# Optimization experiments

Hardware: AMD Instinct MI355X
Metric: run time of the kernel (lower is better)

The kernel has to match this reference:

```python
import jax, jax.numpy as jnp
import numpy as np
from jax import lax

B, W, L, E, V, C, H, O = 16384, 5, 20, 50, 100000, 128, 4096, 50


def setup_inputs() -> dict:
    key = jax.random.key(0)
    ks = jax.random.split(key, 10)
    x = jax.random.randint(ks[0], (B, W), 1, V)
    word_id_to_chars_ids = jax.random.randint(ks[1], (V, L), 0, C)
    word_emb = jax.random.normal(ks[2], (V, E), dtype=jnp.float32) * 0.1
    word_emb = word_emb.at[0].set(0.0)  # padding_idx=0
    char_emb = jax.random.normal(ks[3], (C, E), dtype=jnp.float32) * 0.1
    char_emb = char_emb.at[0].set(0.0)  # padding_idx=0
    conv_w = jax.random.normal(ks[4], (E, E, 3), dtype=jnp.float32) * (1.0 / np.sqrt(E * 3))
    conv_b = jax.random.normal(ks[5], (E,), dtype=jnp.float32) * 0.01
    fc1_w = jax.random.normal(ks[6], (H, E * W), dtype=jnp.float32) * (1.0 / np.sqrt(E * W))
    fc1_b = jnp.zeros((H,), dtype=jnp.float32)
    fc2_w = jax.random.normal(ks[7], (O, H), dtype=jnp.float32) * (1.0 / np.sqrt(H))
    fc2_b = jnp.zeros((O,), dtype=jnp.float32)
    return {"x": x, "word_id_to_chars_ids": word_id_to_chars_ids,
            "word_emb": word_emb, "char_emb": char_emb,
            "conv_w": conv_w, "conv_b": conv_b,
            "fc1_w": fc1_w, "fc1_b": fc1_b, "fc2_w": fc2_w, "fc2_b": fc2_b}


def reference(x, word_id_to_chars_ids, word_emb, char_emb, conv_w, conv_b,
              fc1_w, fc1_b, fc2_w, fc2_b):
    # per-window char ids: [B, 5, L] -> char embeddings [B, 5, L, E]
    char_ids = word_id_to_chars_ids[x]
    ce = char_emb[char_ids]
    # conv1d over char positions: reshape to NCW = [B*5, E, L]
    ce = ce.reshape(B * W, L, E).transpose(0, 2, 1)
    conv = lax.conv_general_dilated(ce, conv_w, window_strides=(1,),
                                    padding=[(1, 1)],
                                    dimension_numbers=("NCH", "OIH", "NCH"))
    conv = conv + conv_b[None, :, None]
    # max-pool over char positions (kernel == L): [B*5, E] -> [B, 5, E]
    chars = jnp.max(conv, axis=2).reshape(B, W, E)
    words = word_emb[x]  # [B, 5, E]
    h = (words + chars).reshape(B, W * E)  # view(-1, 250)
    h = jnp.tanh(h @ fc1_w.T + fc1_b)
    logits = h @ fc2_w.T + fc2_b
    return jax.nn.softmax(logits, axis=1)
```

## Files before the change

kernel.cpp:

```cpp
#include <hip/hip_runtime.h>
#include <hip/hip_bf16.h>


typedef __attribute__((ext_vector_type(8))) short short8;
typedef __attribute__((ext_vector_type(4))) float float4v;

__device__ inline short bf16b(float f) {
    __hip_bfloat16 h = __float2bfloat16(f);
    return *reinterpret_cast<short*>(&h);
}
__device__ inline uint packbf2(float a, float b) {
    return (uint)(ushort)bf16b(a) | ((uint)(ushort)bf16b(b) << 16);
}
__device__ inline void gload_lds16(const void* g, void* l) {
    __builtin_amdgcn_global_load_lds(
        (const __attribute__((address_space(1))) unsigned int*)g,
        (__attribute__((address_space(3))) unsigned int*)l, 16, 0, 0);
}

__global__ __launch_bounds__(256) void prep_kernel(
    const float* __restrict__ fc1_w, const float* __restrict__ fc1_b,
    const float* __restrict__ fc2_w, const float* __restrict__ char_emb,
    const float* __restrict__ conv_w, short* __restrict__ wbf,
    short* __restrict__ w2bf, float* __restrict__ gt2)
{
    const int bid = blockIdx.x;
    if (bid < 4096) {
        int idx = bid * 256 + threadIdx.x;
        int n = idx >> 8, k = idx & 255;
        float v = (k < 250) ? fc1_w[n * 250 + k] : (k == 250 ? fc1_b[n] : 0.f);
        int CT = n >> 4, mm = n & 15;
        int ks = k >> 5, qq = (k >> 3) & 3, j = k & 7;
        wbf[((CT * 8 + ks) * 64 + qq * 16 + mm) * 8 + j] = bf16b(v);
    } else if (bid < 5120) {
        int idx = (bid - 4096) * 256 + threadIdx.x;
        int o = idx >> 12, k = idx & 4095;
        float v = (o < 50) ? fc2_w[idx] : 0.f;
        int Ot = o >> 4, mm = o & 15;
        int kst = k >> 5, qq = (k >> 3) & 3, j = k & 7;
        w2bf[((kst * 4 + Ot) * 64 + qq * 16 + mm) * 8 + j] = bf16b(v);
    } else {
        int idx = (bid - 5120) * 256 + threadIdx.x;
        if (idx >= 19200) return;
        int c = idx / 150, rem = idx - c * 150;
        int kk = rem / 50, o = rem - kk * 50;
        const float* ce = char_emb + c * 50;
        const float* w  = conv_w + o * 150 + kk;
        float s = 0.f;
        #pragma unroll 10
        for (int i = 0; i < 50; ++i) s += ce[i] * w[i * 3];
        if (kk < 2) gt2[(c * 50 + o) * 2 + kk] = s;
        else        gt2[12800 + c * 50 + o] = s;
    }
}

__global__ __launch_bounds__(512, 1) void fused_kernel(
    const int* __restrict__ x, const int* __restrict__ wci,
    const float* __restrict__ word_emb, const float* __restrict__ conv_b,
    const float* __restrict__ gt2, const short* __restrict__ wbf,
    const short* __restrict__ w2bf, const float* __restrict__ fc2_b,
    float* __restrict__ out)
{
    __shared__ char smem[147456];
    short8* Bsv   = (short8*)smem;
    char*   hsb   = smem + 131072;
    float*  partf = (float*)smem;
    char*   gsb   = smem;
    uint*   cpackS = (uint*)(smem + 76800);
    int*    xsS    = (int*)(smem + 83200);
    char*   haS    = smem + 98304;

    const int tid  = threadIdx.x;
    const int lane = tid & 63;
    const int wv   = tid >> 6;
    const int wr = wv >> 2, wc = wv & 3;
    const int q = lane >> 4, m = lane & 15;
    const int m0 = blockIdx.x * 64;
    const int q2base = q >> 1, slot = q & 1;

    const short8* wbfv  = (const short8*)wbf;
    const short8* w2bfv = (const short8*)w2bf;

    {
        const float4* g4 = (const float4*)gt2;
        float4* s4 = (float4*)gsb;
        #pragma unroll
        for (int i = 0; i < 10; ++i) {
            int idx = i * 512 + tid;
            if (idx < 4800) s4[idx] = g4[idx];
        }
    }
    if (tid < 320) {
        const int xid = x[m0 * 5 + tid];
        xsS[tid] = xid;
        const int* crow = wci + (size_t)xid * 20;
        int cid[20];
        #pragma unroll
        for (int p = 0; p < 20; ++p) cid[p] = crow[p];
        #pragma unroll
        for (int u = 0; u < 5; ++u)
            cpackS[tid * 5 + u] = (uint)cid[u * 4] | ((uint)cid[u * 4 + 1] << 8)
                                | ((uint)cid[u * 4 + 2] << 16) | ((uint)cid[u * 4 + 3] << 24);
    }
    __syncthreads();

    {
        const int oc = (lane < 50) ? lane : 49;
        const float cbias = conv_b[oc];
        const int oc8 = oc * 8, oc4 = oc * 4;
        for (int i = 0; i < 40; ++i) {
            const int w = i * 8 + wv;
            const int xid = xsS[w];
            const float wer = word_emb[(size_t)xid * 50 + oc];
            uint cw[5];
            #pragma unroll
            for (int u = 0; u < 5; ++u) cw[u] = cpackS[w * 5 + u];
            int cc[20];
            #pragma unroll
            for (int p = 0; p < 20; ++p)
                cc[p] = (int)((cw[p >> 2] >> ((p & 3) * 8)) & 0xFF);

            float2 r01[11]; float r2[11];
            #pragma unroll
            for (int l = 0; l < 11; ++l) {
                r01[l] = *(const float2*)(gsb + cc[l] * 400 + oc8);
                r2[l]  = *(const float*)(gsb + 51200 + cc[l] * 200 + oc4);
            }
            float mx = r01[0].y + r2[1];
            #pragma unroll
            for (int l = 1; l < 10; ++l) {
                float s = r01[l].y + r01[l - 1].x + r2[l + 1];
                mx = fmaxf(mx, s);
            }
            const float2 r9 = r01[9], r10 = r01[10];

            float2 q01[9]; float q2v[9];
            #pragma unroll
            for (int l = 0; l < 9; ++l) {
                q01[l] = *(const float2*)(gsb + cc[11 + l] * 400 + oc8);
                q2v[l] = *(const float*)(gsb + 51200 + cc[11 + l] * 200 + oc4);
            }
            { float s = r10.y + r9.x + q2v[0];  mx = fmaxf(mx, s); }
            { float s = q01[0].y + r10.x + q2v[1]; mx = fmaxf(mx, s); }
            #pragma unroll
            for (int l = 12; l < 19; ++l) {
                float s = q01[l - 11].y + q01[l - 12].x + q2v[l - 10];
                mx = fmaxf(mx, s);
            }
            { float s = q01[8].y + q01[7].x; mx = fmaxf(mx, s); }

            if (lane < 50) {
                const int s = w / 5, wp = w - s * 5;
                const int byteoff = (s * 512 + (wp * 50 + oc) * 2) ^ ((s & 7) << 4);
                *(short*)(haS + byteoff) = bf16b(mx + cbias + wer);
            }
        }
    }
    if (tid < 384) {
        const int s = tid / 6, j = tid - s * 6;
        const int byteoff = (s * 512 + (250 + j) * 2) ^ ((s & 7) << 4);
        *(short*)(haS + byteoff) = bf16b(j == 0 ? 1.f : 0.f);
    }
    __syncthreads();

    short8 av[2][8];
    #pragma unroll
    for (int mt = 0; mt < 2; ++mt)
        #pragma unroll
        for (int ks = 0; ks < 8; ++ks) {
            const int r = wr * 32 + mt * 16 + m;
            const int byteoff = (r * 512 + ks * 64 + q * 16) ^ ((r & 7) << 4);
            av[mt][ks] = *(const short8*)(haS + byteoff);
        }
    #pragma unroll
    for (int mt = 0; mt < 2; ++mt)
        #pragma unroll
        for (int ks = 0; ks < 8; ++ks)
            asm volatile("" : "+v"(av[mt][ks]));
    __syncthreads();

    #pragma unroll
    for (int i = 0; i < 8; ++i)
        gload_lds16(wbfv + i * 512 + tid, Bsv + i * 512 + tid);
    __syncthreads();

    float4v acc2[2][4] = {};

    #pragma unroll 4
    for (int chg = 0; chg < 32; ++chg) {
        const int buf = chg & 1;

        short8 b2[4];
        #pragma unroll
        for (int Ot = 0; Ot < 4; ++Ot)
            b2[Ot] = w2bfv[(size_t)((chg * 4 + wc) * 4 + Ot) * 64 + lane];

        #pragma unroll
        for (int i = 0; i < 8; ++i)
            gload_lds16(wbfv + (size_t)(chg + 1) * 4096 + i * 512 + tid,
                        Bsv + (buf ^ 1) * 4096 + i * 512 + tid);

        float4v acc[2][2] = {};
        #pragma unroll
        for (int ks = 0; ks < 8; ++ks) {
            short8 bv[2];
            #pragma unroll
            for (int nt = 0; nt < 2; ++nt)
                bv[nt] = Bsv[buf * 4096 + ((wc * 2 + nt) * 8 + ks) * 64 + lane];
            #pragma unroll
            for (int mt = 0; mt < 2; ++mt)
                #pragma unroll
                for (int nt = 0; nt < 2; ++nt)
                    acc[mt][nt] = __builtin_amdgcn_mfma_f32_16x16x32_bf16(
                        bv[nt], av[mt][ks], acc[mt][nt], 0, 0, 0);
        }

        #pragma unroll
        for (int mt = 0; mt < 2; ++mt) {
            const int frag = (wr * 2 + mt) * 4 + wc;
            #pragma unroll
            for (int nt = 0; nt < 2; ++nt) {
                float tv[4];
                #pragma unroll
                for (int r = 0; r < 4; ++r)
                    tv[r] = 1.f - 2.f / (__expf(2.f * acc[mt][nt][r]) + 1.f);
                const int q2 = nt * 2 + q2base;
                const uint p0 = packbf2(tv[0], tv[1]);
                const uint p1 = packbf2(tv[2], tv[3]);
                *(uint2*)(hsb + ((frag * 64 + q2 * 16 + m) * 16 + slot * 8))
                    = make_uint2(p0, p1);
            }
        }

        {
            short8 a2[2];
            #pragma unroll
            for (int mt = 0; mt < 2; ++mt)
                a2[mt] = *(const short8*)(hsb
                    + (((wr * 2 + mt) * 4 + wc) * 64 + lane) * 16);
            #pragma unroll
            for (int mt = 0; mt < 2; ++mt)
                #pragma unroll
                for (int Ot = 0; Ot < 4; ++Ot)
                    acc2[mt][Ot] = __builtin_amdgcn_mfma_f32_16x16x32_bf16(
                        a2[mt], b2[Ot], acc2[mt][Ot], 0, 0, 0);
        }

        __syncthreads();
    }

    #pragma unroll
    for (int mt = 0; mt < 2; ++mt)
        #pragma unroll
        for (int Ot = 0; Ot < 4; ++Ot)
            #pragma unroll
            for (int r = 0; r < 4; ++r)
                partf[(size_t)wc * 4096
                      + ((wr * 2 + mt) * 16 + q * 4 + r) * 64 + Ot * 16 + m]
                    = acc2[mt][Ot][r];
    __syncthreads();

    #pragma unroll
    for (int t = 0; t < 8; ++t) {
        int idx = t * 512 + tid;
        int col = idx & 63;
        float lg = partf[idx] + partf[4096 + idx]
                 + partf[8192 + idx] + partf[12288 + idx];
        partf[idx] = (col < 50) ? lg + fc2_b[col] : -1e30f;
    }
    __syncthreads();

    #pragma unroll
    for (int rr = 0; rr < 8; ++rr) {
        const int row = wv * 8 + rr;
        float v = partf[row * 64 + lane];
        float mx = v;
        #pragma unroll
        for (int off = 32; off > 0; off >>= 1) mx = fmaxf(mx, __shfl_xor(mx, off));
        float e = __expf(v - mx);
        float s = e;
        #pragma unroll
        for (int off = 32; off > 0; off >>= 1) s += __shfl_xor(s, off);
        if (lane < 50)
            out[(size_t)(m0 + row) * 50 + lane] = e / s;
    }
}

extern "C" void kernel_launch(void* const* d_in, const int* in_sizes, int n_in,
                              void* d_out, int out_size, void* d_ws, size_t ws_size,
                              hipStream_t stream) {
    const int*   x        = (const int*)  d_in[0];
    const int*   wci      = (const int*)  d_in[1];
    const float* word_emb = (const float*)d_in[2];
    const float* char_emb = (const float*)d_in[3];
    const float* conv_w   = (const float*)d_in[4];
    const float* conv_b   = (const float*)d_in[5];
    const float* fc1_w    = (const float*)d_in[6];
    const float* fc1_b    = (const float*)d_in[7];
    const float* fc2_w    = (const float*)d_in[8];
    const float* fc2_b    = (const float*)d_in[9];
    float* out = (float*)d_out;

    char* ws = (char*)d_ws;
    short* wbf  = (short*)(ws + ((size_t)8  << 20));
    short* w2bf = (short*)(ws + ((size_t)10 << 20));
    float* gt2  = (float*)(ws + ((size_t)11 << 20));

    prep_kernel<<<5195, 256, 0, stream>>>(fc1_w, fc1_b, fc2_w, char_emb,
                                          conv_w, wbf, w2bf, gt2);
    fused_kernel<<<256, 512, 0, stream>>>(x, wci, word_emb, conv_b, gt2,
                                          wbf, w2bf, fc2_b, out);
}
```

Measured before the change: 193.0 us.

## Pack conv taps as float4 table, batch word_emb loads, overlap fc1 weight prefetch

The precomputed char-conv tap table changes from a float2-plus-float array to one padded float4 per (char, out-channel), so each char position needs a single 16-byte LDS read instead of two. Word-embedding global loads are hoisted and batched eight words at a time, which hides their latency behind the LDS gather work. The first fc1 weight tile prefetch into LDS is issued before the activation reads from LDS, and one barrier is dropped. This moves the LDS region offsets and enlarges the table by a third, which raises LDS footprint and load traffic.

Measured after the change: 192.7 us. Within noise of the previous version (-0.2%).

```diff
diff --git a/kernel.cpp b/kernel.cpp
--- a/kernel.cpp
+++ b/kernel.cpp
@@ -22,7 +22,7 @@
     const float* __restrict__ fc1_w, const float* __restrict__ fc1_b,
     const float* __restrict__ fc2_w, const float* __restrict__ char_emb,
     const float* __restrict__ conv_w, short* __restrict__ wbf,
-    short* __restrict__ w2bf, float* __restrict__ gt2)
+    short* __restrict__ w2bf, float* __restrict__ gt3)
 {
     const int bid = blockIdx.x;
     if (bid < 4096) {
@@ -49,15 +49,15 @@
         float s = 0.f;
         #pragma unroll 10
         for (int i = 0; i < 50; ++i) s += ce[i] * w[i * 3];
-        if (kk < 2) gt2[(c * 50 + o) * 2 + kk] = s;
-        else        gt2[12800 + c * 50 + o] = s;
+        gt3[(c * 50 + o) * 4 + kk] = s;
+        if (kk == 2) gt3[(c * 50 + o) * 4 + 3] = 0.f;
     }
 }
 
 __global__ __launch_bounds__(512, 1) void fused_kernel(
     const int* __restrict__ x, const int* __restrict__ wci,
     const float* __restrict__ word_emb, const float* __restrict__ conv_b,
-    const float* __restrict__ gt2, const short* __restrict__ wbf,
+    const float* __restrict__ gt3, const short* __restrict__ wbf,
     const short* __restrict__ w2bf, const float* __restrict__ fc2_b,
     float* __restrict__ out)
 {
@@ -66,9 +66,9 @@
     char*   hsb   = smem + 131072;
     float*  partf = (float*)smem;
     char*   gsb   = smem;
-    uint*   cpackS = (uint*)(smem + 76800);
-    int*    xsS    = (int*)(smem + 83200);
-    char*   haS    = smem + 98304;
+    uint*   cpackS = (uint*)(smem + 102400);
+    int*    xsS    = (int*)(smem + 108800);
+    char*   haS    = smem + 110080;
 
     const int tid  = threadIdx.x;
     const int lane = tid & 63;
@@ -82,12 +82,12 @@
     const short8* w2bfv = (const short8*)w2bf;
 
     {
-        const float4* g4 = (const float4*)gt2;
+        const float4* g4 = (const float4*)gt3;
         float4* s4 = (float4*)gsb;
         #pragma unroll
-        for (int i = 0; i < 10; ++i) {
+        for (int i = 0; i < 13; ++i) {
             int idx = i * 512 + tid;
-            if (idx < 4800) s4[idx] = g4[idx];
+            if (idx < 6400) s4[idx] = g4[idx];
         }
     }
     if (tid < 320) {
@@ -107,52 +107,53 @@
     {
         const int oc = (lane < 50) ? lane : 49;
         const float cbias = conv_b[oc];
-        const int oc8 = oc * 8, oc4 = oc * 4;
-        for (int i = 0; i < 40; ++i) {
-            const int w = i * 8 + wv;
-            const int xid = xsS[w];
-            const float wer = word_emb[(size_t)xid * 50 + oc];
-            uint cw[5];
-            #pragma unroll
-            for (int u = 0; u < 5; ++u) cw[u] = cpackS[w * 5 + u];
-            int cc[20];
-            #pragma unroll
-            for (int p = 0; p < 20; ++p)
-                cc[p] = (int)((cw[p >> 2] >> ((p & 3) * 8)) & 0xFF);
-
-            float2 r01[11]; float r2[11];
-            #pragma unroll
-            for (int l = 0; l < 11; ++l) {
-                r01[l] = *(const float2*)(gsb + cc[l] * 400 + oc8);
-                r2[l]  = *(const float*)(gsb + 51200 + cc[l] * 200 + oc4);
+        const int oc16 = oc * 16;
+        for (int g = 0; g < 5; ++g) {
+            float werv[8];
+            #pragma unroll
+            for (int j = 0; j < 8; ++j) {
+                const int w = (g * 8 + j) * 8 + wv;
+                werv[j] = word_emb[(size_t)xsS[w] * 50 + oc];
             }
-            float mx = r01[0].y + r2[1];
-            #pragma unroll
-            for (int l = 1; l < 10; ++l) {
-                float s = r01[l].y + r01[l - 1].x + r2[l + 1];
-                mx = fmaxf(mx, s);
-            }
-            const float2 r9 = r01[9], r10 = r01[10];
-
-            float2 q01[9]; float q2v[9];
-            #pragma unroll
-            for (int l = 0; l < 9; ++l) {
-                q01[l] = *(const float2*)(gsb + cc[11 + l] * 400 + oc8);
-                q2v[l] = *(const float*)(gsb + 51200 + cc[11 + l] * 200 + oc4);
-            }
-            { float s = r10.y + r9.x + q2v[0];  mx = fmaxf(mx, s); }
-            { float s = q01[0].y + r10.x + q2v[1]; mx = fmaxf(mx, s); }
-            #pragma unroll
-            for (int l = 12; l < 19; ++l) {
-                float s = q01[l - 11].y + q01[l - 12].x + q2v[l - 10];
-                mx = fmaxf(mx, s);
-            }
-            { float s = q01[8].y + q01[7].x; mx = fmaxf(mx, s); }
-
-            if (lane < 50) {
-                const int s = w / 5, wp = w - s * 5;
-                const int byteoff = (s * 512 + (wp * 50 + oc) * 2) ^ ((s & 7) << 4);
-                *(short*)(haS + byteoff) = bf16b(mx + cbias + wer);
+            #pragma unroll
+            for (int j = 0; j < 8; ++j) {
+                const int w = (g * 8 + j) * 8 + wv;
+                uint cw[5];
+                #pragma unroll
+                for (int u = 0; u < 5; ++u) cw[u] = cpackS[w * 5 + u];
+                int cb[20];
+                #pragma unroll
+                for (int p = 0; p < 20; ++p) {
+                    const int c = (int)((cw[p >> 2] >> ((p & 3) * 8)) & 0xFF);
+                    cb[p] = c * 800 + oc16;
+                }
+                float4 r[11];
+                #pragma unroll
+                for (int l = 0; l < 11; ++l) r[l] = *(const float4*)(gsb + cb[l]);
+                float mx = r[0].y + r[1].z;
+                #pragma unroll
+                for (int l = 1; l < 10; ++l) {
+                    float s = r[l].y + r[l - 1].x + r[l + 1].z;
+                    mx = fmaxf(mx, s);
+                }
+                const float4 r9 = r[9], r10 = r[10];
+                float4 qv[9];
+                #pragma unroll
+                for (int l = 0; l < 9; ++l) qv[l] = *(const float4*)(gsb + cb[11 + l]);
+                { float s = r10.y + r9.x + qv[0].z;    mx = fmaxf(mx, s); }
+                { float s = qv[0].y + r10.x + qv[1].z; mx = fmaxf(mx, s); }
+                #pragma unroll
+                for (int l = 12; l < 19; ++l) {
+                    float s = qv[l - 11].y + qv[l - 12].x + qv[l - 10].z;
+                    mx = fmaxf(mx, s);
+                }
+                { float s = qv[8].y + qv[7].x; mx = fmaxf(mx, s); }
+
+                if (lane < 50) {
+                    const int s = w / 5, wp = w - s * 5;
+                    const int byteoff = (s * 512 + (wp * 50 + oc) * 2) ^ ((s & 7) << 4);
+                    *(short*)(haS + byteoff) = bf16b(mx + cbias + werv[j]);
+                }
             }
         }
     }
@@ -163,6 +164,10 @@
     }
     __syncthreads();
 
+    #pragma unroll
+    for (int i = 0; i < 8; ++i)
+        gload_lds16(wbfv + i * 512 + tid, Bsv + i * 512 + tid);
+
     short8 av[2][8];
     #pragma unroll
     for (int mt = 0; mt < 2; ++mt)
@@ -177,11 +182,6 @@
         #pragma unroll
         for (int ks = 0; ks < 8; ++ks)
             asm volatile("" : "+v"(av[mt][ks]));
-    __syncthreads();
-
-    #pragma unroll
-    for (int i = 0; i < 8; ++i)
-        gload_lds16(wbfv + i * 512 + tid, Bsv + i * 512 + tid);
     __syncthreads();
 
     float4v acc2[2][4] = {};
@@ -304,10 +304,10 @@
     char* ws = (char*)d_ws;
     short* wbf  = (short*)(ws + ((size_t)8  << 20));
     short* w2bf = (short*)(ws + ((size_t)10 << 20));
-    float* gt2  = (float*)(ws + ((size_t)11 << 20));
+    float* gt3  = (float*)(ws + ((size_t)11 << 20));
 
     prep_kernel<<<5195, 256, 0, stream>>>(fc1_w, fc1_b, fc2_w, char_emb,
-                                          conv_w, wbf, w2bf, gt2);
-    fused_kernel<<<256, 512, 0, stream>>>(x, wci, word_emb, conv_b, gt2,
+                                          conv_w, wbf, w2bf, gt3);
+    fused_kernel<<<256, 512, 0, stream>>>(x, wci, word_emb, conv_b, gt3,
                                           wbf, w2bf, fc2_b, out);
 }
```
